# Performance work log

Measured on AMD Instinct MI355X. Metric: run time of the kernel, lower is better.

The kernel has to match this reference:

```python
import jax, jax.numpy as jnp
import numpy as np

K = 512      # model dim (= per-head dim in this module)
HEADS = 8
EPS = 1e-5


def layer_norm_2d(x, scale, offset):
    # haiku LayerNorm(axis=[-2,-1]): normalize over last two axes, per-feature params
    mean = jnp.mean(x, axis=(-2, -1), keepdims=True)
    var = jnp.var(x, axis=(-2, -1), keepdims=True)
    return scale * (x - mean) * jax.lax.rsqrt(var + EPS) + offset


def setup_inputs() -> dict:
    key = jax.random.key(0)
    ks = jax.random.split(key, 10)
    B, T, k, h = 4, 2048, K, HEADS
    s = lambda fan_in: 1.0 / np.sqrt(fan_in)
    return {
        "x": jax.random.normal(ks[0], (B, T, k), dtype=jnp.float32),
        "Wq": jax.random.normal(ks[1], (k, k * h), dtype=jnp.float32) * s(k),
        "Wk": jax.random.normal(ks[2], (k, k * h), dtype=jnp.float32) * s(k),
        "Wv": jax.random.normal(ks[3], (k, k * h), dtype=jnp.float32) * s(k),
        "Wu": jax.random.normal(ks[4], (k * h, k), dtype=jnp.float32) * s(k * h),
        "bu": jnp.zeros((k,), dtype=jnp.float32),
        "ln1_scale": jnp.ones((k,), dtype=jnp.float32),
        "ln1_offset": jnp.zeros((k,), dtype=jnp.float32),
        "W1": jax.random.normal(ks[5], (k, 4 * k), dtype=jnp.float32) * s(k),
        "b1": jnp.zeros((4 * k,), dtype=jnp.float32),
        "W2": jax.random.normal(ks[6], (4 * k, k), dtype=jnp.float32) * s(4 * k),
        "b2": jnp.zeros((k,), dtype=jnp.float32),
        "ln2_scale": jnp.ones((k,), dtype=jnp.float32),
        "ln2_offset": jnp.zeros((k,), dtype=jnp.float32),
    }


def reference(x, Wq, Wk, Wv, Wu, bu, ln1_scale, ln1_offset,
              W1, b1, W2, b2, ln2_scale, ln2_offset):
    B, T, k = x.shape
    h = HEADS
    # projections; '(k h)' split: head index is the FAST axis -> reshape (.., k, h)
    q = (x @ Wq).reshape(B, T, k, h)
    kk = (x @ Wk).reshape(B, T, k, h)
    v = (x @ Wv).reshape(B, T, k, h)
    scale = k ** (-0.25)
    q = q * scale
    kk = kk * scale
    # scores [B, h, T, T]
    dot = jnp.einsum('btkh,bskh->bhts', q, kk)
    dot = jax.nn.softmax(dot, axis=-1)
    # out '(b h) t k -> b t (h k)'
    out = jnp.einsum('bhts,bskh->bthk', dot, v).reshape(B, T, h * k)
    attn = out @ Wu + bu
    x = layer_norm_2d(attn, ln1_scale, ln1_offset) + x
    fwd = jax.nn.gelu(x @ W1 + b1)   # inference mode: dropout = 0
    fwd = fwd @ W2 + b2
    return layer_norm_2d(fwd + x, ln2_scale, ln2_offset)
```

## Files before the change

kernel.cpp:

```cpp
#include <hip/hip_runtime.h>
#include <cstdint>
#include <cstddef>

typedef uint16_t u16;
typedef uint32_t u32;
typedef __bf16 bf16x8 __attribute__((ext_vector_type(8)));
typedef float f32x4 __attribute__((ext_vector_type(4)));

#define TBLK 2048
#define KD 512
#define NH 8
#define MROWS 8192
#define CM 4096

__device__ __forceinline__ u16 f2b(float f){
  u32 u = __builtin_bit_cast(u32, f);
  u = (u + 0x7fffu + ((u >> 16) & 1u)) >> 16;
  return (u16)u;
}

__device__ __forceinline__ float gelu_tanh(float x){
  float x3 = x*x*x;
  float t = tanhf(0.7978845608028654f*(x + 0.044715f*x3));
  return 0.5f*x*(1.0f + t);
}

__device__ __forceinline__ void glds16(const u16* g, u16* l){
  __builtin_amdgcn_global_load_lds((const __attribute__((address_space(1))) void*)g,
                                   (__attribute__((address_space(3))) void*)l,
                                   16, 0, 0);
}

__global__ void to_bf16_kernel(const float* __restrict__ in, u16* __restrict__ out, int n4){
  int i = blockIdx.x*256 + threadIdx.x;
  if (i >= n4) return;
  size_t base = (size_t)i*4;
  float4 v = *(const float4*)(in + base);
  uint2 pk;
  pk.x = (u32)f2b(v.x) | ((u32)f2b(v.y) << 16);
  pk.y = (u32)f2b(v.z) | ((u32)f2b(v.w) << 16);
  *(uint2*)(out + base) = pk;
}

template<bool PERM>
__global__ void transpose_to_bf16(const float* __restrict__ in, u16* __restrict__ out, int R, int C){
  __shared__ float tile[64][65];
  int bc = blockIdx.x*64, br = blockIdx.y*64;
  int tx = threadIdx.x & 63, ty = threadIdx.x >> 6;
  #pragma unroll
  for (int i = 0; i < 64; i += 4)
    tile[ty+i][tx] = in[(size_t)(br+ty+i)*C + bc + tx];
  __syncthreads();
  #pragma unroll
  for (int i = 0; i < 64; i += 4){
    int n = bc + ty + i;
    int np = PERM ? ((n & 7)*512 + (n >> 3)) : n;
    out[(size_t)np*R + br + tx] = f2b(tile[tx][ty+i]);
  }
}

template<int MODE, int BN>
__launch_bounds__(256, 2)
__global__ void gemm_bf16(const u16* __restrict__ A, int lda,
                          const u16* __restrict__ Bt, int M, int N, int K,
                          const float* __restrict__ bias, const float* __restrict__ resid,
                          float scale, u16* __restrict__ out16, float* __restrict__ out32,
                          u16* __restrict__ o2_16 = nullptr, u16* __restrict__ o3_16 = nullptr)
{
  __shared__ alignas(16) u16 At[2][128*32];
  __shared__ alignas(16) u16 Bs[2][BN*32];
  constexpr int MT = (BN == 128) ? 4 : 2;
  constexpr int BU = (BN == 128) ? 2 : 1;
  int ntn = N / BN;
  int tm = blockIdx.x / ntn;
  int tn = blockIdx.x - tm*ntn;
  int m0 = tm << 7, n0 = tn*BN;
  int tid = threadIdx.x;
  int lane = tid & 63;
  int w = tid >> 6;
  int wr = (BN == 128) ? (w >> 1) : w;
  int wc = (BN == 128) ? (w & 1) : 0;
  int rl = lane & 15, gr = lane >> 4;
  int srow = lane >> 2;
  int scol = (lane & 3) ^ ((lane >> 3) & 3);

  f32x4 acc[MT][4];
  #pragma unroll
  for (int m = 0; m < MT; ++m)
    #pragma unroll
    for (int n = 0; n < 4; ++n)
      #pragma unroll
      for (int r = 0; r < 4; ++r) acc[m][n][r] = 0.f;

  auto stage = [&](int buf, int k0){
    #pragma unroll
    for (int i = 0; i < 2; ++i){
      int u = w*2 + i;
      glds16(A + (size_t)(m0 + u*16 + srow)*lda + k0 + scol*8, &At[buf][u*512]);
    }
    #pragma unroll
    for (int i = 0; i < BU; ++i){
      int u = w*BU + i;
      glds16(Bt + (size_t)(n0 + u*16 + srow)*K + k0 + scol*8, &Bs[buf][u*512]);
    }
  };

  stage(0, 0);
  int nsteps = K >> 5;
  for (int s = 0; s < nsteps; ++s){
    int cur = s & 1;
    __syncthreads();
    if (s + 1 < nsteps) stage(cur ^ 1, (s + 1)*32);
    bf16x8 af[MT], bfv[4];
    #pragma unroll
    for (int m = 0; m < MT; ++m){
      int row = wr*MT*16 + m*16 + rl;
      af[m] = *(const bf16x8*)(&At[cur][row*32 + ((gr ^ ((row >> 1) & 3))*8)]);
    }
    #pragma unroll
    for (int n = 0; n < 4; ++n){
      int row = wc*64 + n*16 + rl;
      bfv[n] = *(const bf16x8*)(&Bs[cur][row*32 + ((gr ^ ((row >> 1) & 3))*8)]);
    }
    __builtin_amdgcn_s_setprio(1);
    #pragma unroll
    for (int m = 0; m < MT; ++m)
      #pragma unroll
      for (int n = 0; n < 4; ++n)
        acc[m][n] = __builtin_amdgcn_mfma_f32_16x16x32_bf16(af[m], bfv[n], acc[m][n], 0, 0, 0);
    __builtin_amdgcn_s_setprio(0);
  }

  #pragma unroll
  for (int m = 0; m < MT; ++m){
    #pragma unroll
    for (int n = 0; n < 4; ++n){
      int col = n0 + wc*64 + n*16 + rl;
      #pragma unroll
      for (int r = 0; r < 4; ++r){
        int row = m0 + wr*MT*16 + m*16 + gr*4 + r;
        float v = acc[m][n][r];
        if (MODE == 0){
          out16[(size_t)row*N + col] = f2b(v*scale);
        } else if (MODE == 2){
          out32[(size_t)row*512 + col] = v + bias[col];
        } else if (MODE == 3){
          out16[(size_t)row*2048 + col] = f2b(gelu_tanh(v + bias[col]));
        } else if (MODE == 4){
          out32[(size_t)row*512 + col] = v + bias[col] + resid[(size_t)row*512 + col];
        } else {
          u16* dst = (col < 4096) ? out16 : (col < 8192 ? o2_16 : o3_16);
          float sc = (col < 8192) ? scale : 1.0f;
          dst[(size_t)row*4096 + (col & 4095)] = f2b(v*sc);
        }
      }
    }
  }
}

__global__ void vtrans_kernel(const u16* __restrict__ vg, u16* __restrict__ vtb){
  __shared__ alignas(16) u16 tile[64][72];
  int t0 = blockIdx.x*64;
  int d0 = blockIdx.y*64;
  int bh = blockIdx.z;
  int bl = bh >> 3, h = bh & 7;
  int tid = threadIdx.x;
  #pragma unroll
  for (int it = 0; it < 4; ++it){
    int id = it*256 + tid;
    int r = id >> 4, cq = id & 15;
    *(uint2*)(&tile[r][cq*4]) =
        *(const uint2*)(vg + (size_t)(bl*TBLK + t0 + r)*4096 + h*512 + d0 + cq*4);
  }
  __syncthreads();
  #pragma unroll
  for (int it = 0; it < 2; ++it){
    int id = it*256 + tid;
    int dr = id >> 3, tg = id & 7;
    alignas(16) u16 tmp[8];
    #pragma unroll
    for (int j = 0; j < 8; ++j) tmp[j] = tile[tg*8 + j][dr];
    *(uint4*)(vtb + ((size_t)bh*512 + d0 + dr)*TBLK + t0 + tg*8) = *(const uint4*)tmp;
  }
}

__launch_bounds__(512, 2)
__global__ void flash_attn(const u16* __restrict__ qg, const u16* __restrict__ kg,
                           const u16* __restrict__ vtb, u16* __restrict__ ctx)
{
  int bh = blockIdx.x;
  int qt = blockIdx.y;
  int bl = bh >> 3, h = bh & 7;
  int tid = threadIdx.x;
  int lane = tid & 63, w = tid >> 6;
  int rl = lane & 15, gr = lane >> 4;
  const u16* Qb = qg + (size_t)bl*TBLK*4096 + h*512;
  const u16* Kb = kg + (size_t)bl*TBLK*4096 + h*512;
  const u16* Vb = vtb + (size_t)bh*512*TBLK;

  __shared__ alignas(16) u16 Ka[2][32*512];
  __shared__ alignas(16) u16 Va[2][512*32];
  __shared__ alignas(16) u16 Pl[8][512];

  int q0 = qt*128 + w*16;
  bf16x8 qf[16];
  #pragma unroll
  for (int kc = 0; kc < 16; ++kc)
    qf[kc] = *(const bf16x8*)(Qb + (size_t)(q0 + rl)*4096 + kc*32 + gr*8);

  f32x4 o[32];
  #pragma unroll
  for (int n = 0; n < 32; ++n)
    #pragma unroll
    for (int r = 0; r < 4; ++r) o[n][r] = 0.f;
  float mrow[4] = {-1e30f, -1e30f, -1e30f, -1e30f};
  float lsum[4] = {0.f, 0.f, 0.f, 0.f};

  auto stage = [&](int buf, int s0){
    #pragma unroll
    for (int i = 0; i < 4; ++i){
      int wl = w*4 + i;
      glds16(Kb + (size_t)(s0 + wl)*4096 + (size_t)((lane ^ (wl & 7))*8),
             &Ka[buf][wl*512]);
      int d = wl*16 + (lane >> 2);
      int oj = (lane & 3) ^ ((d >> 1) & 3);
      glds16(Vb + (size_t)d*TBLK + s0 + oj*8,
             &Va[buf][wl*512]);
    }
  };

  stage(0, 0);

  for (int t = 0; t < 64; ++t){
    int cur = t & 1;
    __syncthreads();
    if (t < 63) stage(cur ^ 1, (t + 1)*32);

    f32x4 sA[2];
    #pragma unroll
    for (int n = 0; n < 2; ++n)
      #pragma unroll
      for (int r = 0; r < 4; ++r) sA[n][r] = 0.f;
    __builtin_amdgcn_s_setprio(1);
    #pragma unroll
    for (int kc = 0; kc < 16; ++kc){
      #pragma unroll
      for (int n = 0; n < 2; ++n){
        int rowS = n*16 + rl;
        bf16x8 kf = *(const bf16x8*)(&Ka[cur][rowS*512 + (((kc*4 + gr) ^ (rowS & 7))*8)]);
        sA[n] = __builtin_amdgcn_mfma_f32_16x16x32_bf16(qf[kc], kf, sA[n], 0, 0, 0);
      }
    }
    __builtin_amdgcn_s_setprio(0);

    bool updl = false;
    #pragma unroll
    for (int n = 0; n < 2; ++n)
      #pragma unroll
      for (int r = 0; r < 4; ++r) updl |= (sA[n][r] > mrow[r] + 8.0f);
    if (__any(updl)){
      float pm[4], fr[4];
      #pragma unroll
      for (int r = 0; r < 4; ++r) pm[r] = fmaxf(sA[0][r], sA[1][r]);
      #pragma unroll
      for (int m = 1; m < 16; m <<= 1)
        #pragma unroll
        for (int r = 0; r < 4; ++r) pm[r] = fmaxf(pm[r], __shfl_xor(pm[r], m));
      #pragma unroll
      for (int r = 0; r < 4; ++r){
        float mn = fmaxf(mrow[r], pm[r]);
        fr[r] = __expf(mrow[r] - mn);
        mrow[r] = mn;
        lsum[r] *= fr[r];
      }
      #pragma unroll
      for (int n = 0; n < 32; ++n)
        #pragma unroll
        for (int r = 0; r < 4; ++r) o[n][r] *= fr[r];
    }

    float p0[4], p1[4];
    #pragma unroll
    for (int r = 0; r < 4; ++r){
      p0[r] = __expf(sA[0][r] - mrow[r]);
      p1[r] = __expf(sA[1][r] - mrow[r]);
      lsum[r] += p0[r] + p1[r];
    }

    u16* pw = &Pl[w][0];
    #pragma unroll
    for (int r = 0; r < 4; ++r){
      int tq = gr*4 + r;
      pw[tq*32 + rl]      = f2b(p0[r]);
      pw[tq*32 + 16 + rl] = f2b(p1[r]);
    }
    asm volatile("s_waitcnt lgkmcnt(0)" ::: "memory");
    bf16x8 pa = *(const bf16x8*)(pw + rl*32 + gr*8);

    __builtin_amdgcn_s_setprio(1);
    #pragma unroll
    for (int n = 0; n < 32; ++n){
      int rowV = n*16 + rl;
      bf16x8 vf = *(const bf16x8*)(&Va[cur][rowV*32 + ((gr ^ ((rowV >> 1) & 3))*8)]);
      o[n] = __builtin_amdgcn_mfma_f32_16x16x32_bf16(pa, vf, o[n], 0, 0, 0);
    }
    __builtin_amdgcn_s_setprio(0);
  }

  #pragma unroll
  for (int m = 1; m < 16; m <<= 1)
    #pragma unroll
    for (int r = 0; r < 4; ++r) lsum[r] += __shfl_xor(lsum[r], m);

  #pragma unroll
  for (int n = 0; n < 32; ++n){
    int d = n*16 + rl;
    #pragma unroll
    for (int r = 0; r < 4; ++r){
      int tq = q0 + gr*4 + r;
      float v = o[n][r] / lsum[r];
      ctx[((size_t)(bl*TBLK + tq))*4096 + h*512 + d] = f2b(v);
    }
  }
}

__global__ void reduce_ms(const float* __restrict__ in, float* __restrict__ part, int nblk){
  int b = blockIdx.y;
  const float4* p = (const float4*)(in + (size_t)b*TBLK*KD);
  int n4 = TBLK*KD/4;
  float s = 0.f, s2 = 0.f;
  for (int i = blockIdx.x*blockDim.x + threadIdx.x; i < n4; i += nblk*blockDim.x){
    float4 v = p[i];
    s  += v.x + v.y + v.z + v.w;
    s2 += v.x*v.x + v.y*v.y + v.z*v.z + v.w*v.w;
  }
  #pragma unroll
  for (int m = 1; m < 64; m <<= 1){ s += __shfl_xor(s, m); s2 += __shfl_xor(s2, m); }
  __shared__ float sh[8];
  int w = threadIdx.x >> 6;
  if ((threadIdx.x & 63) == 0){ sh[w] = s; sh[4 + w] = s2; }
  __syncthreads();
  if (threadIdx.x == 0){
    float a = 0.f, a2 = 0.f;
    for (int i = 0; i < 4; ++i){ a += sh[i]; a2 += sh[4 + i]; }
    part[((size_t)b*nblk + blockIdx.x)*2]     = a;
    part[((size_t)b*nblk + blockIdx.x)*2 + 1] = a2;
  }
}

__global__ void finalize_ms(const float* __restrict__ part, float* __restrict__ stats, int nblk){
  int b = blockIdx.x;
  float s = 0.f, s2 = 0.f;
  for (int i = threadIdx.x; i < nblk; i += 64){
    s  += part[((size_t)b*nblk + i)*2];
    s2 += part[((size_t)b*nblk + i)*2 + 1];
  }
  #pragma unroll
  for (int m = 1; m < 64; m <<= 1){ s += __shfl_xor(s, m); s2 += __shfl_xor(s2, m); }
  if (threadIdx.x == 0){
    float inv_n = 1.0f/((float)TBLK*KD);
    float mean = s*inv_n;
    float var = s2*inv_n - mean*mean;
    stats[b*2] = mean;
    stats[b*2 + 1] = 1.0f/sqrtf(var + 1e-5f);
  }
}

__global__ void ln1_apply(const float* __restrict__ attn, const float* __restrict__ x,
                          const float* __restrict__ stats, const float* __restrict__ gs,
                          const float* __restrict__ go, float* __restrict__ x1f,
                          u16* __restrict__ x1b){
  int g = blockIdx.x*256 + threadIdx.x;
  size_t base = (size_t)g*4;
  int b = (int)(base >> 20);
  int col = (int)(base & (KD - 1));
  float mean = stats[b*2], inv = stats[b*2 + 1];
  float4 a  = *(const float4*)(attn + base);
  float4 xr = *(const float4*)(x + base);
  float4 sc = *(const float4*)(gs + col);
  float4 of = *(const float4*)(go + col);
  float4 r;
  r.x = sc.x*(a.x - mean)*inv + of.x + xr.x;
  r.y = sc.y*(a.y - mean)*inv + of.y + xr.y;
  r.z = sc.z*(a.z - mean)*inv + of.z + xr.z;
  r.w = sc.w*(a.w - mean)*inv + of.w + xr.w;
  *(float4*)(x1f + base) = r;
  uint2 pk;
  pk.x = (u32)f2b(r.x) | ((u32)f2b(r.y) << 16);
  pk.y = (u32)f2b(r.z) | ((u32)f2b(r.w) << 16);
  *(uint2*)(x1b + base) = pk;
}

__global__ void ln2_apply(const float* __restrict__ y, const float* __restrict__ stats,
                          const float* __restrict__ gs, const float* __restrict__ go,
                          float* __restrict__ outp){
  int g = blockIdx.x*256 + threadIdx.x;
  size_t base = (size_t)g*4;
  int b = (int)(base >> 20);
  int col = (int)(base & (KD - 1));
  float mean = stats[b*2], inv = stats[b*2 + 1];
  float4 v  = *(const float4*)(y + base);
  float4 sc = *(const float4*)(gs + col);
  float4 of = *(const float4*)(go + col);
  float4 r;
  r.x = sc.x*(v.x - mean)*inv + of.x;
  r.y = sc.y*(v.y - mean)*inv + of.y;
  r.z = sc.z*(v.z - mean)*inv + of.z;
  r.w = sc.w*(v.w - mean)*inv + of.w;
  *(float4*)(outp + base) = r;
}

extern "C" void kernel_launch(void* const* d_in, const int* in_sizes, int n_in,
                              void* d_out, int out_size, void* d_ws, size_t ws_size,
                              hipStream_t stream)
{
  const float* x  = (const float*)d_in[0];
  const float* Wq = (const float*)d_in[1];
  const float* Wk = (const float*)d_in[2];
  const float* Wv = (const float*)d_in[3];
  const float* Wu = (const float*)d_in[4];
  const float* bu = (const float*)d_in[5];
  const float* g1 = (const float*)d_in[6];
  const float* o1 = (const float*)d_in[7];
  const float* W1 = (const float*)d_in[8];
  const float* b1 = (const float*)d_in[9];
  const float* W2 = (const float*)d_in[10];
  const float* b2 = (const float*)d_in[11];
  const float* g2 = (const float*)d_in[12];
  const float* o2 = (const float*)d_in[13];
  float* outp = (float*)d_out;

  char* ws = (char*)d_ws;
  size_t off = 0;
  auto take = [&](size_t bytes)->char*{
    char* p = ws + off; off += (bytes + 255) & ~(size_t)255; return p;
  };
  u16* x16 = (u16*)take((size_t)MROWS*KD*2);
  u16* wqt = (u16*)take((size_t)4096*512*2);
  u16* wkt = (u16*)take((size_t)4096*512*2);
  u16* wvt = (u16*)take((size_t)4096*512*2);
  u16* wut = (u16*)take((size_t)512*4096*2);
  u16* w1t = (u16*)take((size_t)2048*512*2);
  u16* w2t = (u16*)take((size_t)512*2048*2);
  u16* qg  = (u16*)take((size_t)CM*4096*2);
  u16* kg  = (u16*)take((size_t)CM*4096*2);
  u16* vg  = (u16*)take((size_t)CM*4096*2);
  u16* vtb = (u16*)take((size_t)16*512*TBLK*2);
  float* red = (float*)take((size_t)(2*256*2 + 8)*4);
  float* stats = red + 2*256*2;

  u16* ctx    = vg;
  char* qgc   = (char*)qg;
  float* attn = (float*)qgc;
  float* x1f  = (float*)(qgc + (size_t)8*1024*1024);
  u16*   x1b  = (u16*) (qgc + (size_t)16*1024*1024);
  float* yb   = (float*)(qgc + (size_t)20*1024*1024);
  u16*   fwd  = kg;
  (void)ws_size; (void)in_sizes; (void)n_in; (void)out_size;

  const float qscale = 0.21022410381342865f;

  to_bf16_kernel<<<dim3(4096), dim3(256), 0, stream>>>(x, x16, MROWS*KD/4);
  transpose_to_bf16<true ><<<dim3(64, 8), dim3(256), 0, stream>>>(Wq, wqt, 512, 4096);
  transpose_to_bf16<true ><<<dim3(64, 8), dim3(256), 0, stream>>>(Wk, wkt, 512, 4096);
  transpose_to_bf16<true ><<<dim3(64, 8), dim3(256), 0, stream>>>(Wv, wvt, 512, 4096);
  transpose_to_bf16<false><<<dim3(8, 64), dim3(256), 0, stream>>>(Wu, wut, 4096, 512);
  transpose_to_bf16<false><<<dim3(32, 8), dim3(256), 0, stream>>>(W1, w1t, 512, 2048);
  transpose_to_bf16<false><<<dim3(8, 32), dim3(256), 0, stream>>>(W2, w2t, 2048, 512);

  for (int chunk = 0; chunk < 2; ++chunk){
    const u16* xc  = x16 + (size_t)chunk*CM*KD;
    const float* xf = x  + (size_t)chunk*CM*KD;

    gemm_bf16<5,128><<<dim3(32*96), dim3(256), 0, stream>>>(xc, 512, wqt, CM, 12288, 512,
                                                        nullptr, nullptr, qscale, qg, nullptr,
                                                        kg, vg);
    vtrans_kernel<<<dim3(32, 8, 16), dim3(256), 0, stream>>>(vg, vtb);
    flash_attn<<<dim3(16, 16), dim3(512), 0, stream>>>(qg, kg, vtb, ctx);

    gemm_bf16<2,64><<<dim3(32*8), dim3(256), 0, stream>>>(ctx, 4096, wut, CM, 512, 4096,
                                                       bu, nullptr, 1.0f, nullptr, attn);
    reduce_ms<<<dim3(256, 2), dim3(256), 0, stream>>>(attn, red, 256);
    finalize_ms<<<dim3(2), dim3(64), 0, stream>>>(red, stats, 256);
    ln1_apply<<<dim3(2048), dim3(256), 0, stream>>>(attn, xf, stats, g1, o1, x1f, x1b);

    gemm_bf16<3,128><<<dim3(32*16), dim3(256), 0, stream>>>(x1b, 512, w1t, CM, 2048, 512,
                                                        b1, nullptr, 1.0f, fwd, nullptr);
    gemm_bf16<4,64><<<dim3(32*8), dim3(256), 0, stream>>>(fwd, 2048, w2t, CM, 512, 2048,
                                                       b2, x1f, 1.0f, nullptr, yb);
    reduce_ms<<<dim3(256, 2), dim3(256), 0, stream>>>(yb, red, 256);
    finalize_ms<<<dim3(2), dim3(64), 0, stream>>>(red, stats, 256);
    ln2_apply<<<dim3(2048), dim3(256), 0, stream>>>(yb, stats, g2, o2, outp + (size_t)chunk*CM*KD);
  }
}
```

Before: 917.8 us.

## Process all batches in one chunk when workspace allows and reorder attention prefetch

Sizes the processing chunk at run time from the workspace size. When enough scratch exists it handles all 8192 rows in one pass instead of two, so each launch gets twice the blocks (flash attention grid grows from 16 to 32 batch-heads). The next K/V tile prefetch in flash attention now starts after the QK MFMA loop instead of before it. The three QKV weight transposes are merged into one launch. This trades a larger workspace for fewer launches and better GPU fill; the moved prefetch gives less overlap time before the tile is needed.

```diff
diff --git a/kernel.cpp b/kernel.cpp
--- a/kernel.cpp
+++ b/kernel.cpp
@@ -11,7 +11,6 @@
 #define KD 512
 #define NH 8
 #define MROWS 8192
-#define CM 4096
 
 __device__ __forceinline__ u16 f2b(float f){
   u32 u = __builtin_bit_cast(u32, f);
@@ -56,6 +55,26 @@
     int n = bc + ty + i;
     int np = PERM ? ((n & 7)*512 + (n >> 3)) : n;
     out[(size_t)np*R + br + tx] = f2b(tile[tx][ty+i]);
+  }
+}
+
+__global__ void transpose_qkv3(const float* __restrict__ wq, const float* __restrict__ wk,
+                               const float* __restrict__ wv, u16* __restrict__ oq,
+                               u16* __restrict__ ok, u16* __restrict__ ov){
+  __shared__ float tile[64][65];
+  const float* in = (blockIdx.z == 0) ? wq : (blockIdx.z == 1 ? wk : wv);
+  u16* out = (blockIdx.z == 0) ? oq : (blockIdx.z == 1 ? ok : ov);
+  int bc = blockIdx.x*64, br = blockIdx.y*64;
+  int tx = threadIdx.x & 63, ty = threadIdx.x >> 6;
+  #pragma unroll
+  for (int i = 0; i < 64; i += 4)
+    tile[ty+i][tx] = in[(size_t)(br+ty+i)*4096 + bc + tx];
+  __syncthreads();
+  #pragma unroll
+  for (int i = 0; i < 64; i += 4){
+    int n = bc + ty + i;
+    int np = (n & 7)*512 + (n >> 3);
+    out[(size_t)np*512 + br + tx] = f2b(tile[tx][ty+i]);
   }
 }
 
@@ -234,7 +253,6 @@
   for (int t = 0; t < 64; ++t){
     int cur = t & 1;
     __syncthreads();
-    if (t < 63) stage(cur ^ 1, (t + 1)*32);
 
     f32x4 sA[2];
     #pragma unroll
@@ -252,6 +270,8 @@
       }
     }
     __builtin_amdgcn_s_setprio(0);
+
+    if (t < 63) stage(cur ^ 1, (t + 1)*32);
 
     bool updl = false;
     #pragma unroll
@@ -429,6 +449,7 @@
   const float* g2 = (const float*)d_in[12];
   const float* o2 = (const float*)d_in[13];
   float* outp = (float*)d_out;
+  (void)in_sizes; (void)n_in; (void)out_size;
 
   char* ws = (char*)d_ws;
   size_t off = 0;
@@ -442,54 +463,59 @@
   u16* wut = (u16*)take((size_t)512*4096*2);
   u16* w1t = (u16*)take((size_t)2048*512*2);
   u16* w2t = (u16*)take((size_t)512*2048*2);
-  u16* qg  = (u16*)take((size_t)CM*4096*2);
-  u16* kg  = (u16*)take((size_t)CM*4096*2);
-  u16* vg  = (u16*)take((size_t)CM*4096*2);
-  u16* vtb = (u16*)take((size_t)16*512*TBLK*2);
-  float* red = (float*)take((size_t)(2*256*2 + 8)*4);
-  float* stats = red + 2*256*2;
+  float* red = (float*)take((size_t)(4*256*2 + 8)*4);
+  float* stats = red + 4*256*2;
+  size_t fixed_end = off;
+
+  size_t need1 = fixed_end + 4*((size_t)8192*8192 + 256);
+  int cm = (ws_size >= need1) ? 8192 : 4096;
+  int nchunks = MROWS / cm;
+  size_t big = (size_t)cm*8192;
+  u16* qg  = (u16*)take(big);
+  u16* kg  = (u16*)take(big);
+  u16* vg  = (u16*)take(big);
+  u16* vtb = (u16*)take(big);
 
   u16* ctx    = vg;
   char* qgc   = (char*)qg;
   float* attn = (float*)qgc;
-  float* x1f  = (float*)(qgc + (size_t)8*1024*1024);
-  u16*   x1b  = (u16*) (qgc + (size_t)16*1024*1024);
-  float* yb   = (float*)(qgc + (size_t)20*1024*1024);
+  float* x1f  = (float*)(qgc + (size_t)cm*2048);
+  u16*   x1b  = (u16*) (qgc + (size_t)cm*4096);
+  float* yb   = (float*)(qgc + (size_t)cm*5120);
   u16*   fwd  = kg;
-  (void)ws_size; (void)in_sizes; (void)n_in; (void)out_size;
 
   const float qscale = 0.21022410381342865f;
 
   to_bf16_kernel<<<dim3(4096), dim3(256), 0, stream>>>(x, x16, MROWS*KD/4);
-  transpose_to_bf16<true ><<<dim3(64, 8), dim3(256), 0, stream>>>(Wq, wqt, 512, 4096);
-  transpose_to_bf16<true ><<<dim3(64, 8), dim3(256), 0, stream>>>(Wk, wkt, 512, 4096);
-  transpose_to_bf16<true ><<<dim3(64, 8), dim3(256), 0, stream>>>(Wv, wvt, 512, 4096);
+  transpose_qkv3<<<dim3(64, 8, 3), dim3(256), 0, stream>>>(Wq, Wk, Wv, wqt, wkt, wvt);
   transpose_to_bf16<false><<<dim3(8, 64), dim3(256), 0, stream>>>(Wu, wut, 4096, 512);
   transpose_to_bf16<false><<<dim3(32, 8), dim3(256), 0, stream>>>(W1, w1t, 512, 2048);
   transpose_to_bf16<false><<<dim3(8, 32), dim3(256), 0, stream>>>(W2, w2t, 2048, 512);
 
-  for (int chunk = 0; chunk < 2; ++chunk){
-    const u16* xc  = x16 + (size_t)chunk*CM*KD;
-    const float* xf = x  + (size_t)chunk*CM*KD;
-
-    gemm_bf16<5,128><<<dim3(32*96), dim3(256), 0, stream>>>(xc, 512, wqt, CM, 12288, 512,
+  int nb = cm / TBLK;
+  int nbh = nb * NH;
+  for (int chunk = 0; chunk < nchunks; ++chunk){
+    const u16* xc  = x16 + (size_t)chunk*cm*KD;
+    const float* xf = x  + (size_t)chunk*cm*KD;
+
+    gemm_bf16<5,128><<<dim3((cm/128)*96), dim3(256), 0, stream>>>(xc, 512, wqt, cm, 12288, 512,
                                                         nullptr, nullptr, qscale, qg, nullptr,
                                                         kg, vg);
-    vtrans_kernel<<<dim3(32, 8, 16), dim3(256), 0, stream>>>(vg, vtb);
-    flash_attn<<<dim3(16, 16), dim3(512), 0, stream>>>(qg, kg, vtb, ctx);
-
-    gemm_bf16<2,64><<<dim3(32*8), dim3(256), 0, stream>>>(ctx, 4096, wut, CM, 512, 4096,
+    vtrans_kernel<<<dim3(32, 8, nbh), dim3(256), 0, stream>>>(vg, vtb);
+    flash_attn<<<dim3(nbh, 16), dim3(512), 0, stream>>>(qg, kg, vtb, ctx);
+
+    gemm_bf16<2,64><<<dim3((cm/128)*8), dim3(256), 0, stream>>>(ctx, 4096, wut, cm, 512, 4096,
                                                        bu, nullptr, 1.0f, nullptr, attn);
-    reduce_ms<<<dim3(256, 2), dim3(256), 0, stream>>>(attn, red, 256);
-    finalize_ms<<<dim3(2), dim3(64), 0, stream>>>(red, stats, 256);
-    ln1_apply<<<dim3(2048), dim3(256), 0, stream>>>(attn, xf, stats, g1, o1, x1f, x1b);
-
-    gemm_bf16<3,128><<<dim3(32*16), dim3(256), 0, stream>>>(x1b, 512, w1t, CM, 2048, 512,
+    reduce_ms<<<dim3(256, nb), dim3(256), 0, stream>>>(attn, red, 256);
+    finalize_ms<<<dim3(nb), dim3(64), 0, stream>>>(red, stats, 256);
+    ln1_apply<<<dim3(cm/2), dim3(256), 0, stream>>>(attn, xf, stats, g1, o1, x1f, x1b);
+
+    gemm_bf16<3,128><<<dim3((cm/128)*16), dim3(256), 0, stream>>>(x1b, 512, w1t, cm, 2048, 512,
                                                         b1, nullptr, 1.0f, fwd, nullptr);
-    gemm_bf16<4,64><<<dim3(32*8), dim3(256), 0, stream>>>(fwd, 2048, w2t, CM, 512, 2048,
+    gemm_bf16<4,64><<<dim3((cm/128)*8), dim3(256), 0, stream>>>(fwd, 2048, w2t, cm, 512, 2048,
                                                        b2, x1f, 1.0f, nullptr, yb);
-    reduce_ms<<<dim3(256, 2), dim3(256), 0, stream>>>(yb, red, 256);
-    finalize_ms<<<dim3(2), dim3(64), 0, stream>>>(red, stats, 256);
-    ln2_apply<<<dim3(2048), dim3(256), 0, stream>>>(yb, stats, g2, o2, outp + (size_t)chunk*CM*KD);
-  }
-}
+    reduce_ms<<<dim3(256, nb), dim3(256), 0, stream>>>(yb, red, 256);
+    finalize_ms<<<dim3(nb), dim3(64), 0, stream>>>(red, stats, 256);
+    ln2_apply<<<dim3(cm/2), dim3(256), 0, stream>>>(yb, stats, g2, o2, outp + (size_t)chunk*cm*KD);
+  }
+}
```

Result: faster. 867.3 us (-5.5%).
